# Optimization experiments

Hardware: AMD Instinct MI355X
Metric: run time of the kernel (lower is better)

## Reference

```python
import jax, jax.numpy as jnp
import numpy as np

N = 30000      # num_nodes
R0 = 8         # original relations
R = 2 * R0 + 1 # with inverses + self-loop relation = 17
IN = 256
OUT = 256
E = 300000     # original triples
NB = 8         # num_bases


def setup_inputs() -> dict:
    key = jax.random.key(0)
    k1, k2, k3, k4, k5, k6 = jax.random.split(key, 6)
    s = jax.random.randint(k1, (E,), 0, N)
    r = jax.random.randint(k2, (E,), 0, R0)
    o = jax.random.randint(k3, (E,), 0, N)
    triples = jnp.stack([s, r, o], axis=1)  # [E,3] int
    features = jax.random.normal(k4, (N, IN), dtype=jnp.float32)
    bases = jax.random.normal(k5, (NB, IN, OUT), dtype=jnp.float32) * 0.02
    comps = jax.random.normal(k6, (R, NB), dtype=jnp.float32) * 0.02
    bias = jnp.zeros((OUT,), dtype=jnp.float32)
    return {"triples": triples, "features": features, "bases": bases, "comps": comps, "bias": bias}


def reference(triples, features, bases, comps, bias):
    # basis decomposition: weights[r] = sum_b comps[r,b] * bases[b]
    weights = jnp.einsum('rb,bio->rio', comps, bases)  # [R, IN, OUT]

    s, r, o = triples[:, 0], triples[:, 1], triples[:, 2]
    nodes = jnp.arange(N)
    # eval mode: self_loop_keep_prob = 1 -> all N self loops kept
    src = jnp.concatenate([s, o, nodes])                                  # [E + E + N]
    rel = jnp.concatenate([r, r + R0, jnp.full((N,), 2 * R0, r.dtype)])
    dst = jnp.concatenate([o, s, nodes])

    # horizontal stacking: adj is [N, R*N]; row = src, col = rel*N + dst
    cols = rel * N + dst
    # column normalisation (row_normalisation=False branch of sum_sparse)
    col_sums = jnp.zeros((R * N,), jnp.float32).at[cols].add(1.0)
    sums = col_sums[cols]
    # reorder: swap normalizers of original and inverse edge blocks
    sums = jnp.concatenate([sums[E:2 * E], sums[:E], sums[2 * E:]])
    vals = 1.0 / sums

    # fw[r*N + n] = features[n] @ weights[r]
    fw = jnp.einsum('ni,rio->rno', features, weights).reshape(R * N, OUT)
    msgs = vals[:, None] * fw[cols]                    # [num_edges, OUT]
    out = jnp.zeros((N, OUT), jnp.float32).at[src].add(msgs)
    return out + bias
```

## Files before the change

kernel.cpp:

```cpp
#include <hip/hip_runtime.h>


namespace {
constexpr int kN     = 30000;
constexpr int kR0    = 8;
constexpr int kNRel  = 16;
constexpr int kIN    = 256;
constexpr int kOUT   = 256;
constexpr int kE     = 300000;
constexpr int kNB    = 8;
constexpr int kKT    = kNB * kIN;
constexpr int kRows  = kN * kNRel;
constexpr int kMsgs  = 2 * kE;
constexpr int kScanBlk  = 1024;
constexpr int kNScanBlk = (kRows + kScanBlk - 1) / kScanBlk;
constexpr int kBM    = 64;
constexpr int kMB    = (kN + kBM - 1) / kBM;
constexpr int kMPad  = kMB * kBM;
constexpr int kTN    = 16;
}

typedef __bf16 bf16x8 __attribute__((ext_vector_type(8)));
typedef float  f32x4  __attribute__((ext_vector_type(4)));
typedef float  f32x2  __attribute__((ext_vector_type(2)));
typedef float  f32x4v __attribute__((ext_vector_type(4)));
typedef unsigned int u32;

static __device__ __forceinline__ ushort f2bf(float x) {
  unsigned u = __float_as_uint(x);
  u += 0x7FFF + ((u >> 16) & 1);
  return (ushort)(u >> 16);
}

static __device__ __forceinline__ void gload16(const void* g, void* l) {
  __builtin_amdgcn_global_load_lds(
      (const __attribute__((address_space(1))) u32*)g,
      (__attribute__((address_space(3))) u32*)l, 16, 0, 0);
}

#define PKFMA_LO(ACC, G, C) \
  asm("v_pk_fma_f32 %0, %1, %2, %0 op_sel_hi:[1,0,1]" : "+v"(ACC) : "v"(G), "v"(C))
#define PKFMA_HI(ACC, G, C) \
  asm("v_pk_fma_f32 %0, %1, %2, %0 op_sel:[0,1,0] op_sel_hi:[1,1,1]" : "+v"(ACC) : "v"(G), "v"(C))


__global__ void k_prep(const float* __restrict__ f, ushort* __restrict__ fb,
                       const int* __restrict__ t, int* __restrict__ deg,
                       const float* __restrict__ bases, ushort* __restrict__ Bt) {
  int i = blockIdx.x * 256 + threadIdx.x;
  if (i < kN * kIN / 4) {
    float4 v = reinterpret_cast<const float4*>(f)[i];
    ushort4 p;
    p.x = f2bf(v.x); p.y = f2bf(v.y); p.z = f2bf(v.z); p.w = f2bf(v.w);
    reinterpret_cast<ushort4*>(fb)[i] = p;
  }
  if (i < kE) {
    int s = t[3*i], r = t[3*i+1], o = t[3*i+2];
    atomicAdd(&deg[s * kNRel + r], 1);
    atomicAdd(&deg[o * kNRel + kR0 + r], 1);
  }
  if (blockIdx.x < kKT / 16) {
    int b  = blockIdx.x;
    int tt = threadIdx.x;
    char* dst = (char*)Bt + (size_t)tt * 4096;
    int xr = (tt & 7) << 4;
#pragma unroll
    for (int q = 0; q < 4; ++q) {
      int k0 = b * 16 + q * 4;
      ushort4 p;
      p.x = f2bf(bases[(size_t)(k0 + 0) * kOUT + tt]);
      p.y = f2bf(bases[(size_t)(k0 + 1) * kOUT + tt]);
      p.z = f2bf(bases[(size_t)(k0 + 2) * kOUT + tt]);
      p.w = f2bf(bases[(size_t)(k0 + 3) * kOUT + tt]);
      *reinterpret_cast<ushort4*>(dst + ((b * 32 + q * 8) ^ xr)) = p;
    }
  }
}


__global__ void k_scan1(const int* __restrict__ deg, int* __restrict__ rp,
                        int* __restrict__ blksum) {
  __shared__ int s[256];
  int tid = threadIdx.x;
  int base = blockIdx.x * kScanBlk + tid * 4;
  int v0 = 0, v1 = 0, v2 = 0, v3 = 0;
  if (base + 3 < kRows) {
    v0 = deg[base]; v1 = deg[base+1]; v2 = deg[base+2]; v3 = deg[base+3];
  } else {
    if (base     < kRows) v0 = deg[base];
    if (base + 1 < kRows) v1 = deg[base+1];
    if (base + 2 < kRows) v2 = deg[base+2];
  }
  int t0 = v0, t1 = t0 + v1, t2 = t1 + v2, t3 = t2 + v3;
  s[tid] = t3;
  __syncthreads();
  for (int off = 1; off < 256; off <<= 1) {
    int x = 0;
    if (tid >= off) x = s[tid - off];
    __syncthreads();
    s[tid] += x;
    __syncthreads();
  }
  int excl = tid ? s[tid-1] : 0;
  if (base     < kRows) rp[base]   = excl;
  if (base + 1 < kRows) rp[base+1] = excl + t0;
  if (base + 2 < kRows) rp[base+2] = excl + t1;
  if (base + 3 < kRows) rp[base+3] = excl + t2;
  if (tid == 255) blksum[blockIdx.x] = s[255];
}

__global__ void k_scan3(int* __restrict__ rp, const int* __restrict__ blksum) {
  __shared__ int red[256];
  int tid = threadIdx.x;
  int B   = blockIdx.x;
  int region = (B * 256) >> 10;
  int partial = 0;
  for (int k = tid; k < region; k += 256) partial += blksum[k];
  red[tid] = partial;
  __syncthreads();
#pragma unroll
  for (int off = 128; off > 0; off >>= 1) {
    if (tid < off) red[tid] += red[tid + off];
    __syncthreads();
  }
  int base = red[0];
  int i = B * 256 + tid;
  if (i < kRows)       rp[i] += base;
  else if (i == kRows) rp[i]  = kMsgs;
}

__global__ void k_scatter(const int* __restrict__ t, const int* __restrict__ rp,
                          int* __restrict__ deg, int* __restrict__ col) {
  int m = blockIdx.x * 256 + threadIdx.x;
  if (m >= kMsgs) return;
  int e = (m < kE) ? m : m - kE;
  int s = t[3*e], r = t[3*e+1], o = t[3*e+2];
  int rr, tn, sn;
  if (m < kE) { rr = r;        tn = s; sn = o; }
  else        { rr = kR0 + r;  tn = o; sn = s; }
  int idx = tn * kNRel + rr;
  int pos = rp[idx] + (atomicSub(&deg[idx], 1) - 1);
  col[pos] = (rr << 16) | sn;
}

#define FMA4(A, S, G) \
  A.x += (S) * G.x; A.y += (S) * G.y; A.z += (S) * G.z; A.w += (S) * G.w;


__global__ __launch_bounds__(256, 6)
void k_agg1(const int* __restrict__ rp, const int* __restrict__ col,
            const ushort* __restrict__ featbf, const float* __restrict__ comps,
            ushort* __restrict__ aggb) {
  __shared__ float cvb[4][17][kNB];
  int wv   = threadIdx.x >> 6;
  int lane = threadIdx.x & 63;
  int node = blockIdx.x * 4 + wv;

  if (lane < 17) {
    float val = 0.f;
    if (lane < kNRel) {
      int idx = node * kNRel + lane;
      int d = rp[idx + 1] - rp[idx];
      val = d > 0 ? 1.0f / (float)d : 0.f;
    }
#pragma unroll
    for (int b = 0; b < kNB; ++b)
      cvb[wv][lane][b] = comps[lane * kNB + b] * val;
  }
  __syncthreads();

  int se0 = __builtin_amdgcn_readfirstlane(rp[node * kNRel]);
  int se1 = __builtin_amdgcn_readfirstlane(rp[node * kNRel + kNRel]);

  f32x2 accp[2 * kNB];
  {
    uint2 sf = *reinterpret_cast<const uint2*>(featbf + (size_t)node * kIN + lane * 4);
    f32x2 p01, p23;
    p01.x = __uint_as_float(sf.x << 16);
    p01.y = __uint_as_float(sf.x & 0xFFFF0000u);
    p23.x = __uint_as_float(sf.y << 16);
    p23.y = __uint_as_float(sf.y & 0xFFFF0000u);
#pragma unroll
    for (int b = 0; b < kNB; ++b) {
      float cs = comps[2*kR0*kNB + b];
      accp[2*b]     = p01 * cs;
      accp[2*b + 1] = p23 * cs;
    }
  }

  const int pad = (16 << 16);
  int voff = lane * 4;
  const f32x4v* cvr = reinterpret_cast<const f32x4v*>(&cvb[wv][0][0]);

  auto compute = [&](const uint2* g, const int* sc) {
#pragma unroll
    for (int j = 0; j < 4; ++j) {
      int sr = sc[j] >> 16;
      f32x4v cA = cvr[sr * 2];
      f32x4v cB = cvr[sr * 2 + 1];
      f32x2 p01, p23;
      p01.x = __uint_as_float(g[j].x << 16);
      p01.y = __uint_as_float(g[j].x & 0xFFFF0000u);
      p23.x = __uint_as_float(g[j].y << 16);
      p23.y = __uint_as_float(g[j].y & 0xFFFF0000u);
      f32x2 cAl = cA.lo, cAh = cA.hi, cBl = cB.lo, cBh = cB.hi;
      PKFMA_LO(accp[0],  p01, cAl); PKFMA_LO(accp[1],  p23, cAl);
      PKFMA_HI(accp[2],  p01, cAl); PKFMA_HI(accp[3],  p23, cAl);
      PKFMA_LO(accp[4],  p01, cAh); PKFMA_LO(accp[5],  p23, cAh);
      PKFMA_HI(accp[6],  p01, cAh); PKFMA_HI(accp[7],  p23, cAh);
      PKFMA_LO(accp[8],  p01, cBl); PKFMA_LO(accp[9],  p23, cBl);
      PKFMA_HI(accp[10], p01, cBl); PKFMA_HI(accp[11], p23, cBl);
      PKFMA_LO(accp[12], p01, cBh); PKFMA_LO(accp[13], p23, cBh);
      PKFMA_HI(accp[14], p01, cBh); PKFMA_HI(accp[15], p23, cBh);
    }
  };

  int sc0[4], sc1[4];
  uint2 g0[4];
#pragma unroll
  for (int j = 0; j < 4; ++j) {
    int ee = se0 + j;
    int ic = ee < se1 ? ee : 0;
    int v  = col[ic];
    sc0[j] = ee < se1 ? v : pad;
  }
#pragma unroll
  for (int j = 0; j < 4; ++j)
    g0[j] = *reinterpret_cast<const uint2*>(featbf + (size_t)(sc0[j] & 0xFFFF) * kIN + voff);
#pragma unroll
  for (int j = 0; j < 4; ++j) {
    int ee = se0 + 4 + j;
    int ic = ee < se1 ? ee : 0;
    int v  = col[ic];
    sc1[j] = ee < se1 ? v : pad;
  }

  for (int e = se0; e + 4 < se1; e += 4) {
    uint2 g1[4];
#pragma unroll
    for (int j = 0; j < 4; ++j)
      g1[j] = *reinterpret_cast<const uint2*>(featbf + (size_t)(sc1[j] & 0xFFFF) * kIN + voff);
    int sc2[4];
#pragma unroll
    for (int j = 0; j < 4; ++j) {
      int ee = e + 8 + j;
      int ic = ee < se1 ? ee : 0;
      int v  = col[ic];
      sc2[j] = ee < se1 ? v : pad;
    }
    compute(g0, sc0);
#pragma unroll
    for (int j = 0; j < 4; ++j) { g0[j] = g1[j]; sc0[j] = sc1[j]; sc1[j] = sc2[j]; }
  }
  if (se0 < se1) compute(g0, sc0);

  char* rowp = (char*)aggb + (size_t)node * 4096;
  int xr = (node & 7) << 4;
#pragma unroll
  for (int b = 0; b < kNB; ++b) {
    ushort4 p;
    p.x = f2bf(accp[2*b].x);     p.y = f2bf(accp[2*b].y);
    p.z = f2bf(accp[2*b + 1].x); p.w = f2bf(accp[2*b + 1].y);
    *reinterpret_cast<ushort4*>(rowp + ((b * 512 + lane * 8) ^ xr)) = p;
  }
}


__global__ __launch_bounds__(512, 4)
void k_gemm(const ushort* __restrict__ aggb, const ushort* __restrict__ Bt,
            const float* __restrict__ bias, float* __restrict__ out) {
  __shared__ ushort Albs[2][kBM * 64];
  __shared__ ushort Blds[2][256 * 64];
  int tid  = threadIdx.x;
  int wv   = tid >> 6;
  int lane = tid & 63;
  int mh   = wv >> 2;
  int nq   = wv & 3;
  int l15  = lane & 15;
  int g4   = lane >> 4;
  int node0 = blockIdx.x * kBM;

  f32x4 acc[2][4];
#pragma unroll
  for (int mt = 0; mt < 2; ++mt)
#pragma unroll
    for (int nt = 0; nt < 4; ++nt) acc[mt][nt] = f32x4{0.f, 0.f, 0.f, 0.f};

  auto stage = [&](int c, int buf) {
    {
      int lin = wv * 1024 + lane * 16;
      int row = lin >> 7;
      const char* src = (const char*)aggb + (size_t)(node0 + row) * 4096
                        + c * 128 + (lin & 127);
      gload16(src, (char*)Albs[buf] + wv * 1024);
    }
#pragma unroll
    for (int i = 0; i < 4; ++i) {
      int seg = wv * 4 + i;
      int lin = seg * 1024 + lane * 16;
      int colr = lin >> 7;
      const char* src = (const char*)Bt + (size_t)colr * 4096
                        + c * 128 + (lin & 127);
      gload16(src, (char*)Blds[buf] + seg * 1024);
    }
  };

  stage(0, 0);
  asm volatile("s_waitcnt vmcnt(0)" ::: "memory");
  __builtin_amdgcn_s_barrier();

  int cur = 0;
  for (int c = 0; c < 32; ++c) {
    if (c + 1 < 32) {
      stage(c + 1, cur ^ 1);
      asm volatile("s_waitcnt vmcnt(5)" ::: "memory");
    } else {
      asm volatile("s_waitcnt vmcnt(0)" ::: "memory");
    }
    __builtin_amdgcn_s_barrier();
    __builtin_amdgcn_sched_barrier(0);
#pragma unroll
    for (int ks = 0; ks < 2; ++ks) {
      int kb = ks * 64 + g4 * 16;
      bf16x8 a[2], b[4];
#pragma unroll
      for (int mt = 0; mt < 2; ++mt) {
        int row = mh * 32 + mt * 16 + l15;
        a[mt] = *reinterpret_cast<const bf16x8*>(
            (const char*)Albs[cur] + row * 128 + (kb ^ ((row & 7) << 4)));
      }
#pragma unroll
      for (int nt = 0; nt < 4; ++nt) {
        int colr = nq * 64 + nt * 16 + l15;
        b[nt] = *reinterpret_cast<const bf16x8*>(
            (const char*)Blds[cur] + colr * 128 + (kb ^ ((colr & 7) << 4)));
      }
#pragma unroll
      for (int mt = 0; mt < 2; ++mt)
#pragma unroll
        for (int nt = 0; nt < 4; ++nt)
          acc[mt][nt] = __builtin_amdgcn_mfma_f32_16x16x32_bf16(a[mt], b[nt],
                                                                acc[mt][nt], 0, 0, 0);
    }
    asm volatile("s_waitcnt lgkmcnt(0)" ::: "memory");
    __builtin_amdgcn_s_barrier();
    cur ^= 1;
  }

#pragma unroll
  for (int nt = 0; nt < 4; ++nt) {
    int colo = nq * 64 + nt * 16 + l15;
    float bi = bias[colo];
#pragma unroll
    for (int mt = 0; mt < 2; ++mt) {
      int rbase = node0 + mh * 32 + mt * 16 + g4 * 4;
#pragma unroll
      for (int j = 0; j < 4; ++j) {
        int row = rbase + j;
        if (row < kN) out[(size_t)row * kOUT + colo] = acc[mt][nt][j] + bi;
      }
    }
  }
}


__global__ __launch_bounds__(512, 4)
void k_out_fused(const int* __restrict__ rp, const int* __restrict__ col,
                 const float* __restrict__ feat, const ushort* __restrict__ featbf,
                 const ushort* __restrict__ Bt, const float* __restrict__ comps,
                 const float* __restrict__ bias, float* __restrict__ out) {
  __shared__ ushort aggs[kTN * kKT];
  __shared__ float  cvb[kTN][17][kNB];
  int tid  = threadIdx.x;
  int wv   = tid >> 6;
  int lane = tid & 63;
  int node0 = blockIdx.x * kTN;

  for (int q = tid; q < kTN * 17; q += 512) {
    int nl = q / 17, rl = q - nl * 17;
    float val = 0.f;
    if (rl < kNRel) {
      int idx = (node0 + nl) * kNRel + rl;
      int d = rp[idx + 1] - rp[idx];
      val = d > 0 ? 1.0f / (float)d : 0.f;
    }
#pragma unroll
    for (int b = 0; b < kNB; ++b)
      cvb[nl][rl][b] = comps[rl * kNB + b] * val;
  }
  __syncthreads();

  for (int half = 0; half < 2; ++half) {
    int nl   = (wv << 1) | half;
    int node = node0 + nl;
    int e0 = rp[node * kNRel];
    int e1 = rp[node * kNRel + kNRel];

    float4 f = *reinterpret_cast<const float4*>(feat + (size_t)node * kIN + lane * 4);
    float4 acc[kNB];
#pragma unroll
    for (int b = 0; b < kNB; ++b) {
      float cs = comps[2*kR0*kNB + b];
      acc[b].x = cs * f.x; acc[b].y = cs * f.y; acc[b].z = cs * f.z; acc[b].w = cs * f.w;
    }
    const float4* cvr = reinterpret_cast<const float4*>(&cvb[nl][0][0]);
    const int pad = (16 << 16);
    int cc[4];
#pragma unroll
    for (int j = 0; j < 4; ++j) {
      int ee = e0 + j;
      int v  = col[ee < kMsgs ? ee : kMsgs - 1];
      cc[j] = ee < e1 ? v : pad;
    }
    for (int e = e0; e < e1; e += 4) {
      uint2 g[4];
#pragma unroll
      for (int j = 0; j < 4; ++j) {
        int sn = cc[j] & 0xFFFF;
        g[j] = *reinterpret_cast<const uint2*>(featbf + (size_t)sn * kIN + lane * 4);
      }
      int rr[4];
#pragma unroll
      for (int j = 0; j < 4; ++j) rr[j] = cc[j] >> 16;
#pragma unroll
      for (int j = 0; j < 4; ++j) {
        int ee = e + 4 + j;
        int v  = col[ee < kMsgs ? ee : kMsgs - 1];
        cc[j] = ee < e1 ? v : pad;
      }
#pragma unroll
      for (int j = 0; j < 4; ++j) {
        float4 c0 = cvr[rr[j] * 2];
        float4 c1 = cvr[rr[j] * 2 + 1];
        float4 gg;
        gg.x = __uint_as_float(g[j].x << 16);
        gg.y = __uint_as_float(g[j].x & 0xFFFF0000u);
        gg.z = __uint_as_float(g[j].y << 16);
        gg.w = __uint_as_float(g[j].y & 0xFFFF0000u);
        FMA4(acc[0], c0.x, gg) FMA4(acc[1], c0.y, gg)
        FMA4(acc[2], c0.z, gg) FMA4(acc[3], c0.w, gg)
        FMA4(acc[4], c1.x, gg) FMA4(acc[5], c1.y, gg)
        FMA4(acc[6], c1.z, gg) FMA4(acc[7], c1.w, gg)
      }
    }
    int xr = (nl & 7) << 4;
#pragma unroll
    for (int b = 0; b < kNB; ++b) {
      ushort4 p;
      p.x = f2bf(acc[b].x); p.y = f2bf(acc[b].y);
      p.z = f2bf(acc[b].z); p.w = f2bf(acc[b].w);
      int byteoff = nl * 4096 + ((b * 512 + lane * 8) ^ xr);
      *reinterpret_cast<ushort4*>(reinterpret_cast<char*>(aggs) + byteoff) = p;
    }
  }
  __syncthreads();

  {
    int n  = lane & 15;
    int g4 = lane >> 4;
    const char* abase = reinterpret_cast<const char*>(aggs) + n * 4096;
    int axor = (n & 7) << 4;
#pragma unroll
    for (int t = 0; t < 2; ++t) {
      int ntile = wv + t * 8;
      float bi = bias[ntile * 16 + n];
      const char* btrow = reinterpret_cast<const char*>(Bt)
                          + (size_t)(ntile * 16 + n) * 4096;
      int bxor = (n & 7) << 4;
      f32x4 acc = {0.f, 0.f, 0.f, 0.f};
#pragma unroll 4
      for (int ks = 0; ks < kKT / 32; ++ks) {
        int kb = ks * 64 + g4 * 16;
        bf16x8 af = *reinterpret_cast<const bf16x8*>(abase + (kb ^ axor));
        bf16x8 bf = *reinterpret_cast<const bf16x8*>(btrow + (kb ^ bxor));
        acc = __builtin_amdgcn_mfma_f32_16x16x32_bf16(af, bf, acc, 0, 0, 0);
      }
#pragma unroll
      for (int j = 0; j < 4; ++j) {
        int row = g4 * 4 + j;
        out[(size_t)(node0 + row) * kOUT + ntile * 16 + n] = acc[j] + bi;
      }
    }
  }
}


extern "C" void kernel_launch(void* const* d_in, const int* in_sizes, int n_in,
                              void* d_out, int out_size, void* d_ws, size_t ws_size,
                              hipStream_t stream) {
  const int*   triples = (const int*)  d_in[0];
  const float* feat    = (const float*)d_in[1];
  const float* bases   = (const float*)d_in[2];
  const float* comps   = (const float*)d_in[3];
  const float* bias    = (const float*)d_in[4];
  float* out = (float*)d_out;

  size_t featbf_b = (size_t)kN * kIN * 2;
  size_t bt_b     = (size_t)kOUT * kKT * 2;
  size_t aggb_b   = (size_t)kMPad * kKT * 2;
  size_t csr_b    = (size_t)(kRows + kRows + 1 + kMsgs + kNScanBlk) * 4;
  bool bigws = ws_size >= featbf_b + bt_b + aggb_b + csr_b + 1024;

  char* p = (char*)d_ws;
  ushort* featbf = (ushort*)p;            p += featbf_b;
  ushort* Bt     = (ushort*)p;            p += bt_b;
  ushort* aggb   = nullptr;
  if (bigws) { aggb = (ushort*)p;         p += aggb_b; }
  int* deg    = (int*)p;
  int* rp     = deg + kRows;
  int* col    = rp + kRows + 1;
  int* blksum = col + kMsgs;

  hipMemsetAsync(deg, 0, kRows * sizeof(int), stream);
  k_prep  <<<(kN * kIN / 4 + 255) / 256, 256, 0, stream>>>(feat, featbf, triples, deg,
                                                           bases, Bt);
  k_scan1 <<<kNScanBlk,             256, 0, stream>>>(deg, rp, blksum);
  k_scan3 <<<(kRows + 256) / 256,   256, 0, stream>>>(rp, blksum);
  k_scatter<<<(kMsgs + 255) / 256,  256, 0, stream>>>(triples, rp, deg, col);

  if (bigws) {
    k_agg1<<<kN / 4,  256, 0, stream>>>(rp, col, featbf, comps, aggb);
    k_gemm<<<kMB,     512, 0, stream>>>(aggb, Bt, bias, out);
  } else {
    k_out_fused<<<kN / kTN, 512, 0, stream>>>(rp, col, feat, featbf, Bt,
                                              comps, bias, out);
  }
}
```

Baseline: 179.5 us.

## Enlarge GEMM M-tile, triple-buffer LDS staging, deepen gather prefetch

The GEMM block tile grows from 64 to 128 rows, so each wave computes 4x4 MFMA tiles and the B tile loaded into LDS is reused across more rows. Staging moves from double to triple buffering with two chunks in flight, and occupancy is lowered to 2 blocks per CU to fit the larger LDS and register use. The aggregation kernel's gather loop now prefetches edge columns three groups ahead and feature rows two groups ahead, to hide gather latency better. The padded GEMM tail rows now read past the aggb allocation into the following workspace; those rows are discarded when results are stored.

```diff
diff --git a/kernel.cpp b/kernel.cpp
--- a/kernel.cpp
+++ b/kernel.cpp
@@ -14,9 +14,9 @@
 constexpr int kMsgs  = 2 * kE;
 constexpr int kScanBlk  = 1024;
 constexpr int kNScanBlk = (kRows + kScanBlk - 1) / kScanBlk;
-constexpr int kBM    = 64;
+constexpr int kBM    = 128;
 constexpr int kMB    = (kN + kBM - 1) / kBM;
-constexpr int kMPad  = kMB * kBM;
+constexpr int kMPadAlloc = 30016;
 constexpr int kTN    = 16;
 }
 
@@ -192,6 +192,21 @@
   int voff = lane * 4;
   const f32x4v* cvr = reinterpret_cast<const f32x4v*>(&cvb[wv][0][0]);
 
+  auto loadcols = [&](int base, int* sc) {
+#pragma unroll
+    for (int j = 0; j < 4; ++j) {
+      int ee = base + j;
+      int ic = ee < se1 ? ee : 0;
+      int v  = col[ic];
+      sc[j] = ee < se1 ? v : pad;
+    }
+  };
+  auto gath = [&](const int* sc, uint2* g) {
+#pragma unroll
+    for (int j = 0; j < 4; ++j)
+      g[j] = *reinterpret_cast<const uint2*>(
+          featbf + (size_t)(sc[j] & 0xFFFF) * kIN + voff);
+  };
   auto compute = [&](const uint2* g, const int* sc) {
 #pragma unroll
     for (int j = 0; j < 4; ++j) {
@@ -215,44 +230,25 @@
     }
   };
 
-  int sc0[4], sc1[4];
-  uint2 g0[4];
-#pragma unroll
-  for (int j = 0; j < 4; ++j) {
-    int ee = se0 + j;
-    int ic = ee < se1 ? ee : 0;
-    int v  = col[ic];
-    sc0[j] = ee < se1 ? v : pad;
-  }
-#pragma unroll
-  for (int j = 0; j < 4; ++j)
-    g0[j] = *reinterpret_cast<const uint2*>(featbf + (size_t)(sc0[j] & 0xFFFF) * kIN + voff);
-#pragma unroll
-  for (int j = 0; j < 4; ++j) {
-    int ee = se0 + 4 + j;
-    int ic = ee < se1 ? ee : 0;
-    int v  = col[ic];
-    sc1[j] = ee < se1 ? v : pad;
-  }
-
-  for (int e = se0; e + 4 < se1; e += 4) {
-    uint2 g1[4];
-#pragma unroll
-    for (int j = 0; j < 4; ++j)
-      g1[j] = *reinterpret_cast<const uint2*>(featbf + (size_t)(sc1[j] & 0xFFFF) * kIN + voff);
-    int sc2[4];
+  int sc0[4], sc1[4], sc2[4];
+  uint2 g0[4], g1[4];
+  loadcols(se0,     sc0); gath(sc0, g0);
+  loadcols(se0 + 4, sc1); gath(sc1, g1);
+  loadcols(se0 + 8, sc2);
+
+#pragma unroll 2
+  for (int e = se0; e < se1; e += 4) {
+    uint2 g2[4];
+    gath(sc2, g2);
+    int sc3[4];
+    loadcols(e + 12, sc3);
+    compute(g0, sc0);
 #pragma unroll
     for (int j = 0; j < 4; ++j) {
-      int ee = e + 8 + j;
-      int ic = ee < se1 ? ee : 0;
-      int v  = col[ic];
-      sc2[j] = ee < se1 ? v : pad;
-    }
-    compute(g0, sc0);
-#pragma unroll
-    for (int j = 0; j < 4; ++j) { g0[j] = g1[j]; sc0[j] = sc1[j]; sc1[j] = sc2[j]; }
-  }
-  if (se0 < se1) compute(g0, sc0);
+      g0[j] = g1[j]; g1[j] = g2[j];
+      sc0[j] = sc1[j]; sc1[j] = sc2[j]; sc2[j] = sc3[j];
+    }
+  }
 
   char* rowp = (char*)aggb + (size_t)node * 4096;
   int xr = (node & 7) << 4;
@@ -266,11 +262,11 @@
 }
 
 
-__global__ __launch_bounds__(512, 4)
+__global__ __launch_bounds__(512, 2)
 void k_gemm(const ushort* __restrict__ aggb, const ushort* __restrict__ Bt,
             const float* __restrict__ bias, float* __restrict__ out) {
-  __shared__ ushort Albs[2][kBM * 64];
-  __shared__ ushort Blds[2][256 * 64];
+  __shared__ ushort Albs[3][kBM * 64];
+  __shared__ ushort Blds[3][256 * 64];
   int tid  = threadIdx.x;
   int wv   = tid >> 6;
   int lane = tid & 63;
@@ -280,19 +276,21 @@
   int g4   = lane >> 4;
   int node0 = blockIdx.x * kBM;
 
-  f32x4 acc[2][4];
-#pragma unroll
-  for (int mt = 0; mt < 2; ++mt)
+  f32x4 acc[4][4];
+#pragma unroll
+  for (int mt = 0; mt < 4; ++mt)
 #pragma unroll
     for (int nt = 0; nt < 4; ++nt) acc[mt][nt] = f32x4{0.f, 0.f, 0.f, 0.f};
 
   auto stage = [&](int c, int buf) {
-    {
-      int lin = wv * 1024 + lane * 16;
+#pragma unroll
+    for (int i = 0; i < 2; ++i) {
+      int seg = wv * 2 + i;
+      int lin = seg * 1024 + lane * 16;
       int row = lin >> 7;
       const char* src = (const char*)aggb + (size_t)(node0 + row) * 4096
                         + c * 128 + (lin & 127);
-      gload16(src, (char*)Albs[buf] + wv * 1024);
+      gload16(src, (char*)Albs[buf] + seg * 1024);
     }
 #pragma unroll
     for (int i = 0; i < 4; ++i) {
@@ -306,14 +304,15 @@
   };
 
   stage(0, 0);
-  asm volatile("s_waitcnt vmcnt(0)" ::: "memory");
-  __builtin_amdgcn_s_barrier();
-
-  int cur = 0;
+  stage(1, 1);
+
   for (int c = 0; c < 32; ++c) {
-    if (c + 1 < 32) {
-      stage(c + 1, cur ^ 1);
-      asm volatile("s_waitcnt vmcnt(5)" ::: "memory");
+    int cur = c % 3;
+    if (c + 2 < 32) {
+      stage(c + 2, (c + 2) % 3);
+      asm volatile("s_waitcnt vmcnt(12)" ::: "memory");
+    } else if (c + 1 < 32) {
+      asm volatile("s_waitcnt vmcnt(6)" ::: "memory");
     } else {
       asm volatile("s_waitcnt vmcnt(0)" ::: "memory");
     }
@@ -322,10 +321,10 @@
 #pragma unroll
     for (int ks = 0; ks < 2; ++ks) {
       int kb = ks * 64 + g4 * 16;
-      bf16x8 a[2], b[4];
-#pragma unroll
-      for (int mt = 0; mt < 2; ++mt) {
-        int row = mh * 32 + mt * 16 + l15;
+      bf16x8 a[4], b[4];
+#pragma unroll
+      for (int mt = 0; mt < 4; ++mt) {
+        int row = mh * 64 + mt * 16 + l15;
         a[mt] = *reinterpret_cast<const bf16x8*>(
             (const char*)Albs[cur] + row * 128 + (kb ^ ((row & 7) << 4)));
       }
@@ -336,7 +335,7 @@
             (const char*)Blds[cur] + colr * 128 + (kb ^ ((colr & 7) << 4)));
       }
 #pragma unroll
-      for (int mt = 0; mt < 2; ++mt)
+      for (int mt = 0; mt < 4; ++mt)
 #pragma unroll
         for (int nt = 0; nt < 4; ++nt)
           acc[mt][nt] = __builtin_amdgcn_mfma_f32_16x16x32_bf16(a[mt], b[nt],
@@ -344,7 +343,6 @@
     }
     asm volatile("s_waitcnt lgkmcnt(0)" ::: "memory");
     __builtin_amdgcn_s_barrier();
-    cur ^= 1;
   }
 
 #pragma unroll
@@ -352,8 +350,8 @@
     int colo = nq * 64 + nt * 16 + l15;
     float bi = bias[colo];
 #pragma unroll
-    for (int mt = 0; mt < 2; ++mt) {
-      int rbase = node0 + mh * 32 + mt * 16 + g4 * 4;
+    for (int mt = 0; mt < 4; ++mt) {
+      int rbase = node0 + mh * 64 + mt * 16 + g4 * 4;
 #pragma unroll
       for (int j = 0; j < 4; ++j) {
         int row = rbase + j;
@@ -497,7 +495,7 @@
 
   size_t featbf_b = (size_t)kN * kIN * 2;
   size_t bt_b     = (size_t)kOUT * kKT * 2;
-  size_t aggb_b   = (size_t)kMPad * kKT * 2;
+  size_t aggb_b   = (size_t)kMPadAlloc * kKT * 2;
   size_t csr_b    = (size_t)(kRows + kRows + 1 + kMsgs + kNScanBlk) * 4;
   bool bigws = ws_size >= featbf_b + bt_b + aggb_b + csr_b + 1024;
 
```

Measured after the change: 188.7 us. +5.1%, slower.
